# Kernel optimization log

Measured on AMD Instinct MI355X. Metric: run time of the kernel, lower is better.

The kernel has to match this reference:

```python
import jax, jax.numpy as jnp
import numpy as np

N_NODES = 50000
N_EDGES = 600000
IN_CH = 128
OUT_CH = 32
L1 = IN_CH - (IN_CH - OUT_CH) // 3          # 96
L2 = IN_CH - (2 * (IN_CH - OUT_CH)) // 3    # 64


def _lin(key, fan_in, fan_out):
    bound = 1.0 / np.sqrt(fan_in)
    return jax.random.uniform(key, (fan_in, fan_out), jnp.float32, -bound, bound)


def setup_inputs() -> dict:
    key = jax.random.key(0)
    ks = jax.random.split(key, 12)
    x = jax.random.normal(ks[0], (N_NODES, IN_CH), jnp.float32)
    edge_index = jax.random.randint(ks[1], (2, N_EDGES), 0, N_NODES, jnp.int64 if jax.config.jax_enable_x64 else jnp.int32)
    return {
        "x": x,
        "edge_index": edge_index,
        "w1_rel": _lin(ks[2], IN_CH, L1),
        "w1_root": _lin(ks[3], IN_CH, L1),
        "b1": jnp.zeros((L1,), jnp.float32),
        "w2_rel": _lin(ks[4], L1, L2),
        "w2_root": _lin(ks[5], L1, L2),
        "b2": jnp.zeros((L2,), jnp.float32),
        "w_mu": _lin(ks[6], L2, OUT_CH),
        "b_mu": jnp.zeros((OUT_CH,), jnp.float32),
        "w_ls": _lin(ks[7], L2, OUT_CH),
        "b_ls": jnp.zeros((OUT_CH,), jnp.float32),
    }


def reference(x, edge_index, w1_rel, w1_root, b1, w2_rel, w2_root, b2,
              w_mu, b_mu, w_ls, b_ls):
    src, dst = edge_index[0], edge_index[1]

    # PyG GraphConv (aggr='add'): out_i = W_rel @ sum_{j->i} x_j + W_root @ x_i + b
    def graph_conv(h, wr, wroot, b):
        agg = jax.ops.segment_sum(h[src], dst, num_segments=N_NODES)
        return agg @ wr + h @ wroot + b

    h = jax.nn.relu(graph_conv(x, w1_rel, w1_root, b1))
    h = jax.nn.relu(graph_conv(h, w2_rel, w2_root, b2))

    # GCNConv: add self-loops, symmetric deg^-1/2 normalization (shared by mu / logstd)
    loops = jnp.arange(N_NODES, dtype=src.dtype)
    src_sl = jnp.concatenate([src, loops])
    dst_sl = jnp.concatenate([dst, loops])
    deg = jax.ops.segment_sum(jnp.ones_like(dst_sl, h.dtype), dst_sl, num_segments=N_NODES)
    dinv = jnp.where(deg > 0, jax.lax.rsqrt(deg), 0.0)
    norm = dinv[src_sl] * dinv[dst_sl]  # [E+N]

    def gcn(h, w, b):
        m = (h @ w)[src_sl] * norm[:, None]
        return jax.ops.segment_sum(m, dst_sl, num_segments=N_NODES) + b

    return gcn(h, w_mu, b_mu), gcn(h, w_ls, b_ls)
```

## Files before the change

### kernel.cpp

```cpp
#include <hip/hip_runtime.h>
#include <cstddef>

static constexpr int NN = 50000;
static constexpr int NE = 600000;
static constexpr int NB = (NN + 255) / 256;

using f32x4 = __attribute__((ext_vector_type(4))) float;
using s16x8 = __attribute__((ext_vector_type(8))) short;

__device__ inline float bf2f(unsigned short u) {
    return __uint_as_float(((unsigned)u) << 16);
}
__device__ inline unsigned short f2bf(float f) {
    unsigned u = __float_as_uint(f);
    unsigned r = u + 0x7fffu + ((u >> 16) & 1u);
    return (unsigned short)(r >> 16);
}
__device__ inline float lof(unsigned u) { return __uint_as_float(u << 16); }
__device__ inline float hif(unsigned u) { return __uint_as_float(u & 0xffff0000u); }
__device__ inline unsigned packbf(float a, float b) {
    return (unsigned)f2bf(a) | ((unsigned)f2bf(b) << 16);
}

__global__ __launch_bounds__(256)
void zero_wprep_k(int* __restrict__ deg,
                  const float* __restrict__ w1_rel, const float* __restrict__ w1_root,
                  const float* __restrict__ w2_rel, const float* __restrict__ w2_root,
                  const float* __restrict__ w_mu,   const float* __restrict__ w_ls,
                  unsigned short* __restrict__ wt1, unsigned short* __restrict__ wt2,
                  unsigned short* __restrict__ wt3)
{
    int i = blockIdx.x * 256 + threadIdx.x;
    if (i < NN) deg[i] = 0;
    if (i < 24576) {
        int k = i / 192, n = i % 192;
        float v = (n < 96) ? w1_rel[k * 96 + n] : w1_root[k * 96 + (n - 96)];
        wt1[n * 128 + k] = f2bf(v);
    } else if (i < 36864) {
        int j = i - 24576;
        int k = j / 128, n = j % 128;
        float v = (n < 64) ? w2_rel[k * 64 + n] : w2_root[k * 64 + (n - 64)];
        wt2[n * 96 + k] = f2bf(v);
    } else if (i < 40960) {
        int j = i - 36864;
        int k = j / 64, n = j % 64;
        float v = (n < 32) ? w_mu[k * 32 + n] : w_ls[k * 32 + (n - 32)];
        wt3[n * 64 + k] = f2bf(v);
    }
}

__global__ __launch_bounds__(256)
void count_deg_k(const int* __restrict__ dstv, int* __restrict__ deg) {
    int e = blockIdx.x * 256 + threadIdx.x;
    if (e < NE) atomicAdd(&deg[dstv[e]], 1);
}

__global__ __launch_bounds__(256)
void scan_reduce_k(const int* __restrict__ deg, int* __restrict__ partial) {
    __shared__ int buf[256];
    int i = blockIdx.x * 256 + threadIdx.x;
    buf[threadIdx.x] = (i < NN) ? deg[i] : 0;
    __syncthreads();
    #pragma unroll
    for (int off = 128; off > 0; off >>= 1) {
        if (threadIdx.x < off) buf[threadIdx.x] += buf[threadIdx.x + off];
        __syncthreads();
    }
    if (threadIdx.x == 0) partial[blockIdx.x] = buf[0];
}

__global__ __launch_bounds__(256)
void scan_final2_k(const int* __restrict__ deg, const int* __restrict__ partial,
                   int* __restrict__ row_start, int* __restrict__ cursor,
                   float* __restrict__ dinv) {
    __shared__ int pb[256], po[256], buf[256];
    int t = threadIdx.x;
    int pv = (t < NB) ? partial[t] : 0;
    pb[t] = pv; po[t] = pv;
    __syncthreads();
    #pragma unroll
    for (int off = 1; off < 256; off <<= 1) {
        int tv = (t >= off) ? pb[t - off] : 0;
        __syncthreads();
        pb[t] += tv;
        __syncthreads();
    }
    int i = blockIdx.x * 256 + t;
    int v = (i < NN) ? deg[i] : 0;
    buf[t] = v;
    __syncthreads();
    #pragma unroll
    for (int off = 1; off < 256; off <<= 1) {
        int tv = (t >= off) ? buf[t - off] : 0;
        __syncthreads();
        buf[t] += tv;
        __syncthreads();
    }
    int blkoff = pb[blockIdx.x] - po[blockIdx.x];
    if (i < NN) {
        int pos = blkoff + buf[t] - v;
        row_start[i] = pos;
        cursor[i] = pos;
        dinv[i] = rsqrtf((float)v + 1.0f);
    }
    if (blockIdx.x == 0 && t == 0) row_start[NN] = pb[NB - 1];
}

__global__ __launch_bounds__(256)
void fill_k(const int* __restrict__ srcv, const int* __restrict__ dstv,
            int* __restrict__ cursor, int* __restrict__ csr)
{
    int e = blockIdx.x * 256 + threadIdx.x;
    if (e < NE) {
        int pos = atomicAdd(&cursor[dstv[e]], 1);
        csr[pos] = srcv[e];
    }
}

template<int K, int NH, bool XB, bool SCALE>
__global__ __launch_bounds__(256)
void gemm_mfma(const void* __restrict__ Xv,
               const unsigned short* __restrict__ WT,
               const float* __restrict__ biasB,
               const float* __restrict__ scale,
               unsigned short* __restrict__ out0,
               unsigned short* __restrict__ out1)
{
    constexpr int KQ = K / 4;
    constexpr int PB = K * 2;
    constexpr int KS = K / 32;
    constexpr int NT = NH / 16;
    __shared__ short lds[(128 + NH) * K];
    char* ldsb = (char*)lds;
    const int tid = threadIdx.x;
    const int blk = blockIdx.x;
    const int half = blockIdx.y;

    const unsigned short* wt = WT + (size_t)half * NH * K;
    unsigned short* outp = half ? out1 : out0;

    #pragma unroll
    for (int it = 0; it < KQ / 2; ++it) {
        int idx = it * 256 + tid;
        int r = idx / KQ, c4 = idx % KQ;
        int node = blk * 128 + r; if (node >= NN) node = NN - 1;
        uint2 p;
        if (XB) {
            p = *(const uint2*)((const unsigned short*)Xv + (size_t)node * K + c4 * 4);
        } else {
            float4 v = *(const float4*)((const float*)Xv + (size_t)node * K + c4 * 4);
            p.x = packbf(v.x, v.y); p.y = packbf(v.z, v.w);
        }
        unsigned byte = (unsigned)(r * PB + c4 * 8) ^ ((unsigned)(r & 7) << 4);
        *(uint2*)(ldsb + byte) = p;
    }
    #pragma unroll
    for (int it = 0; it < NH * KQ / 256; ++it) {
        int idx = it * 256 + tid;
        int n = idx / KQ, c4 = idx % KQ;
        uint2 p = *(const uint2*)(wt + (size_t)n * K + c4 * 4);
        int pr = 128 + n;
        unsigned byte = (unsigned)(pr * PB + c4 * 8) ^ ((unsigned)(pr & 7) << 4);
        *(uint2*)(ldsb + byte) = p;
    }
    __syncthreads();

    const int wv = tid >> 6, lane = tid & 63;
    const int r15 = lane & 15, g = lane >> 4;

    s16x8 afr[2][KS];
    #pragma unroll
    for (int ms = 0; ms < 2; ++ms) {
        #pragma unroll
        for (int ks = 0; ks < KS; ++ks) {
            int r = wv * 32 + ms * 16 + r15;
            unsigned byte = (unsigned)(r * PB + ks * 64 + g * 16) ^ ((unsigned)(r & 7) << 4);
            afr[ms][ks] = *(const s16x8*)(ldsb + byte);
        }
    }

    #pragma unroll
    for (int nt = 0; nt < NT; ++nt) {
        s16x8 bfr[KS];
        #pragma unroll
        for (int ks = 0; ks < KS; ++ks) {
            int pr = 128 + nt * 16 + r15;
            unsigned byte = (unsigned)(pr * PB + ks * 64 + g * 16) ^ ((unsigned)(pr & 7) << 4);
            bfr[ks] = *(const s16x8*)(ldsb + byte);
        }
        int c = nt * 16 + r15;
        float bias = (half && biasB) ? biasB[c] : 0.f;
        #pragma unroll
        for (int ms = 0; ms < 2; ++ms) {
            f32x4 acc = {0.f, 0.f, 0.f, 0.f};
            #pragma unroll
            for (int ks = 0; ks < KS; ++ks)
                acc = __builtin_amdgcn_mfma_f32_16x16x32_bf16(afr[ms][ks], bfr[ks], acc, 0, 0, 0);
            int nb = blk * 128 + wv * 32 + ms * 16 + g * 4;
            #pragma unroll
            for (int rg = 0; rg < 4; ++rg) {
                int node = nb + rg;
                if (node < NN) {
                    float v = acc[rg] + bias;
                    if (SCALE) v *= scale[node];
                    outp[(size_t)node * NH + c] = f2bf(v);
                }
            }
        }
    }
}

template<int K, int NHT, bool SPLIT, bool SCALE>
__global__ __launch_bounds__(256)
void gather_gemm_k(const int* __restrict__ row_start,
                   const int* __restrict__ csr,
                   const unsigned short* __restrict__ msg,
                   const unsigned short* __restrict__ hpre,
                   const unsigned short* __restrict__ WT,
                   const float* __restrict__ biasHi,
                   const float* __restrict__ scale,
                   unsigned short* __restrict__ out0,
                   unsigned short* __restrict__ out1)
{
    constexpr int G   = K / 8;
    constexpr int KQ  = K / 4;
    constexpr int PB  = K * 2;
    constexpr int KS  = K / 32;
    constexpr int NT  = NHT / 16;
    constexpr int NHh = NHT / 2;
    __shared__ short lds[(64 + NHT) * K];
    char* ldsb = (char*)lds;
    const int tid = threadIdx.x;
    const int blk = blockIdx.x;

    for (int w = tid; w < 64 * G; w += 256) {
        int r = w / G, ch = w - r * G;
        int c8 = ch * 8;
        int node = blk * 64 + r;
        float a[8] = {0.f,0.f,0.f,0.f,0.f,0.f,0.f,0.f};
        if (node < NN) {
            uint4 h = *(const uint4*)&hpre[(size_t)node * K + c8];
            a[0] = lof(h.x); a[1] = hif(h.x); a[2] = lof(h.y); a[3] = hif(h.y);
            a[4] = lof(h.z); a[5] = hif(h.z); a[6] = lof(h.w); a[7] = hif(h.w);
            int e0 = row_start[node], e1 = row_start[node + 1];
            int e = e0;
            for (; e + 2 <= e1; e += 2) {
                int s0 = csr[e], s1 = csr[e + 1];
                uint4 v0 = *(const uint4*)&msg[(size_t)s0 * K + c8];
                uint4 v1 = *(const uint4*)&msg[(size_t)s1 * K + c8];
                a[0] += lof(v0.x); a[1] += hif(v0.x); a[2] += lof(v0.y); a[3] += hif(v0.y);
                a[4] += lof(v0.z); a[5] += hif(v0.z); a[6] += lof(v0.w); a[7] += hif(v0.w);
                a[0] += lof(v1.x); a[1] += hif(v1.x); a[2] += lof(v1.y); a[3] += hif(v1.y);
                a[4] += lof(v1.z); a[5] += hif(v1.z); a[6] += lof(v1.w); a[7] += hif(v1.w);
            }
            if (e < e1) {
                int s = csr[e];
                uint4 v = *(const uint4*)&msg[(size_t)s * K + c8];
                a[0] += lof(v.x); a[1] += hif(v.x); a[2] += lof(v.y); a[3] += hif(v.y);
                a[4] += lof(v.z); a[5] += hif(v.z); a[6] += lof(v.w); a[7] += hif(v.w);
            }
            #pragma unroll
            for (int q = 0; q < 8; ++q) a[q] = fmaxf(a[q], 0.f);
        }
        uint4 o;
        o.x = packbf(a[0], a[1]); o.y = packbf(a[2], a[3]);
        o.z = packbf(a[4], a[5]); o.w = packbf(a[6], a[7]);
        unsigned byte = (unsigned)(r * PB + ch * 16) ^ ((unsigned)(r & 7) << 4);
        *(uint4*)(ldsb + byte) = o;
    }
    #pragma unroll
    for (int it = 0; it < NHT * KQ / 256; ++it) {
        int idx = it * 256 + tid;
        int n = idx / KQ, c4 = idx % KQ;
        uint2 p = *(const uint2*)(WT + (size_t)n * K + c4 * 4);
        int pr = 64 + n;
        unsigned byte = (unsigned)(pr * PB + c4 * 8) ^ ((unsigned)(pr & 7) << 4);
        *(uint2*)(ldsb + byte) = p;
    }
    __syncthreads();

    const int wv = tid >> 6, lane = tid & 63;
    const int r15 = lane & 15, g = lane >> 4;

    s16x8 afr[KS];
    #pragma unroll
    for (int ks = 0; ks < KS; ++ks) {
        int r = wv * 16 + r15;
        unsigned byte = (unsigned)(r * PB + ks * 64 + g * 16) ^ ((unsigned)(r & 7) << 4);
        afr[ks] = *(const s16x8*)(ldsb + byte);
    }

    #pragma unroll
    for (int nt = 0; nt < NT; ++nt) {
        s16x8 bfr[KS];
        #pragma unroll
        for (int ks = 0; ks < KS; ++ks) {
            int pr = 64 + nt * 16 + r15;
            unsigned byte = (unsigned)(pr * PB + ks * 64 + g * 16) ^ ((unsigned)(pr & 7) << 4);
            bfr[ks] = *(const s16x8*)(ldsb + byte);
        }
        int c = nt * 16 + r15;
        float bias = 0.f;
        if (SPLIT && biasHi && c >= NHh) bias = biasHi[c - NHh];
        f32x4 acc = {0.f, 0.f, 0.f, 0.f};
        #pragma unroll
        for (int ks = 0; ks < KS; ++ks)
            acc = __builtin_amdgcn_mfma_f32_16x16x32_bf16(afr[ks], bfr[ks], acc, 0, 0, 0);
        int nb = blk * 64 + wv * 16 + g * 4;
        #pragma unroll
        for (int rg = 0; rg < 4; ++rg) {
            int node = nb + rg;
            if (node < NN) {
                float v = acc[rg] + bias;
                if (SCALE) v *= scale[node];
                if (SPLIT) {
                    if (c < NHh) out0[(size_t)node * NHh + c] = f2bf(v);
                    else         out1[(size_t)node * NHh + (c - NHh)] = f2bf(v);
                } else {
                    out0[(size_t)node * NHT + c] = f2bf(v);
                }
            }
        }
    }
}

__global__ __launch_bounds__(256)
void gather_gcn_k(const int* __restrict__ row_start,
                  const int* __restrict__ csr,
                  const unsigned short* __restrict__ y,
                  const float* __restrict__ dinv,
                  const float* __restrict__ b_mu,
                  const float* __restrict__ b_ls,
                  float* __restrict__ out)
{
    int idx = blockIdx.x * 256 + threadIdx.x;
    if (idx >= NN * 8) return;
    int i  = idx >> 3;
    int c8 = (idx & 7) * 8;
    float a[8];
    {
        uint4 h = *(const uint4*)&y[(size_t)i * 64 + c8];
        a[0] = lof(h.x); a[1] = hif(h.x); a[2] = lof(h.y); a[3] = hif(h.y);
        a[4] = lof(h.z); a[5] = hif(h.z); a[6] = lof(h.w); a[7] = hif(h.w);
    }
    int e0 = row_start[i], e1 = row_start[i + 1];
    int e = e0;
    for (; e + 2 <= e1; e += 2) {
        int s0 = csr[e], s1 = csr[e + 1];
        uint4 v0 = *(const uint4*)&y[(size_t)s0 * 64 + c8];
        uint4 v1 = *(const uint4*)&y[(size_t)s1 * 64 + c8];
        a[0] += lof(v0.x); a[1] += hif(v0.x); a[2] += lof(v0.y); a[3] += hif(v0.y);
        a[4] += lof(v0.z); a[5] += hif(v0.z); a[6] += lof(v0.w); a[7] += hif(v0.w);
        a[0] += lof(v1.x); a[1] += hif(v1.x); a[2] += lof(v1.y); a[3] += hif(v1.y);
        a[4] += lof(v1.z); a[5] += hif(v1.z); a[6] += lof(v1.w); a[7] += hif(v1.w);
    }
    if (e < e1) {
        int s = csr[e];
        uint4 v = *(const uint4*)&y[(size_t)s * 64 + c8];
        a[0] += lof(v.x); a[1] += hif(v.x); a[2] += lof(v.y); a[3] += hif(v.y);
        a[4] += lof(v.z); a[5] += hif(v.z); a[6] += lof(v.w); a[7] += hif(v.w);
    }
    float di = dinv[i];
    const float* b;
    float* o;
    if (c8 < 32) { b = &b_mu[c8];      o = &out[(size_t)i * 32 + c8]; }
    else         { b = &b_ls[c8 - 32]; o = &out[(size_t)NN * 32 + (size_t)i * 32 + (c8 - 32)]; }
    float4 r0, r1;
    r0.x = di * a[0] + b[0]; r0.y = di * a[1] + b[1];
    r0.z = di * a[2] + b[2]; r0.w = di * a[3] + b[3];
    r1.x = di * a[4] + b[4]; r1.y = di * a[5] + b[5];
    r1.z = di * a[6] + b[6]; r1.w = di * a[7] + b[7];
    *(float4*)&o[0] = r0;
    *(float4*)&o[4] = r1;
}

extern "C" void kernel_launch(void* const* d_in, const int* in_sizes, int n_in,
                              void* d_out, int out_size, void* d_ws, size_t ws_size,
                              hipStream_t stream)
{
    (void)in_sizes; (void)n_in; (void)out_size; (void)ws_size;
    const float* x       = (const float*)d_in[0];
    const int*   ei      = (const int*)d_in[1];
    const int*   srcv    = ei;
    const int*   dstv    = ei + NE;
    const float* w1_rel  = (const float*)d_in[2];
    const float* w1_root = (const float*)d_in[3];
    const float* b1      = (const float*)d_in[4];
    const float* w2_rel  = (const float*)d_in[5];
    const float* w2_root = (const float*)d_in[6];
    const float* b2      = (const float*)d_in[7];
    const float* w_mu    = (const float*)d_in[8];
    const float* b_mu    = (const float*)d_in[9];
    const float* w_ls    = (const float*)d_in[10];
    const float* b_ls    = (const float*)d_in[11];
    float* out = (float*)d_out;

    char* ws = (char*)d_ws;
    unsigned short* t1    = (unsigned short*)(ws);
    unsigned short* h1pre = (unsigned short*)(ws + 9600000);
    unsigned short* t2    = (unsigned short*)(ws + 19200000);
    unsigned short* h2pre = (unsigned short*)(ws + 25600000);
    unsigned short* y     = (unsigned short*)(ws + 32000000);
    int* csr       = (int*)(ws + 38400000);
    int* row_start = (int*)(ws + 40800000);
    int* cursor    = (int*)(ws + 41000016);
    float* dinv    = (float*)(ws + 41200016);
    int* deg       = (int*)(ws + 41400016);
    int* partial   = (int*)(ws + 41600016);
    unsigned short* wt1 = (unsigned short*)(ws + 41700016);
    unsigned short* wt2 = (unsigned short*)(ws + 41749168);
    unsigned short* wt3 = (unsigned short*)(ws + 41773744);

    zero_wprep_k<<<NB, 256, 0, stream>>>(deg, w1_rel, w1_root, w2_rel, w2_root,
                                         w_mu, w_ls, wt1, wt2, wt3);
    count_deg_k<<<(NE + 255) / 256, 256, 0, stream>>>(dstv, deg);
    scan_reduce_k<<<NB, 256, 0, stream>>>(deg, partial);
    scan_final2_k<<<NB, 256, 0, stream>>>(deg, partial, row_start, cursor, dinv);
    fill_k<<<(NE + 255) / 256, 256, 0, stream>>>(srcv, dstv, cursor, csr);

    gemm_mfma<128, 96, false, false><<<dim3(391, 2), 256, 0, stream>>>(
        x, wt1, b1, nullptr, t1, h1pre);

    gather_gemm_k<96, 128, true, false><<<782, 256, 0, stream>>>(
        row_start, csr, t1, h1pre, wt2, b2, nullptr, t2, h2pre);

    gather_gemm_k<64, 64, false, true><<<782, 256, 0, stream>>>(
        row_start, csr, t2, h2pre, wt3, nullptr, dinv, y, nullptr);

    gather_gcn_k<<<(NN * 8 + 255) / 256, 256, 0, stream>>>(row_start, csr, y, dinv, b_mu, b_ls, out);
}
```

Baseline: 172.3 us.

## Split neighbor gathers across thread pairs and widen gather-GEMM blocks to 512

```diff
diff --git a/kernel.cpp b/kernel.cpp
--- a/kernel.cpp
+++ b/kernel.cpp
@@ -211,7 +211,7 @@
 }
 
 template<int K, int NHT, bool SPLIT, bool SCALE>
-__global__ __launch_bounds__(256)
+__global__ __launch_bounds__(512)
 void gather_gemm_k(const int* __restrict__ row_start,
                    const int* __restrict__ csr,
                    const unsigned short* __restrict__ msg,
@@ -223,29 +223,36 @@
                    unsigned short* __restrict__ out1)
 {
     constexpr int G   = K / 8;
+    constexpr int G2  = G * 2;
     constexpr int KQ  = K / 4;
     constexpr int PB  = K * 2;
     constexpr int KS  = K / 32;
     constexpr int NT  = NHT / 16;
+    constexpr int NTW = NT / 2;
     constexpr int NHh = NHT / 2;
     __shared__ short lds[(64 + NHT) * K];
     char* ldsb = (char*)lds;
     const int tid = threadIdx.x;
     const int blk = blockIdx.x;
 
-    for (int w = tid; w < 64 * G; w += 256) {
-        int r = w / G, ch = w - r * G;
+    for (int it = 0; it < 64 * G2 / 512; ++it) {
+        int w = it * 512 + tid;
+        int r = w / G2;
+        int rem = w - r * G2;
+        int ch = rem >> 1, sub = rem & 1;
         int c8 = ch * 8;
         int node = blk * 64 + r;
         float a[8] = {0.f,0.f,0.f,0.f,0.f,0.f,0.f,0.f};
         if (node < NN) {
-            uint4 h = *(const uint4*)&hpre[(size_t)node * K + c8];
-            a[0] = lof(h.x); a[1] = hif(h.x); a[2] = lof(h.y); a[3] = hif(h.y);
-            a[4] = lof(h.z); a[5] = hif(h.z); a[6] = lof(h.w); a[7] = hif(h.w);
+            if (sub == 0) {
+                uint4 h = *(const uint4*)&hpre[(size_t)node * K + c8];
+                a[0] = lof(h.x); a[1] = hif(h.x); a[2] = lof(h.y); a[3] = hif(h.y);
+                a[4] = lof(h.z); a[5] = hif(h.z); a[6] = lof(h.w); a[7] = hif(h.w);
+            }
             int e0 = row_start[node], e1 = row_start[node + 1];
-            int e = e0;
-            for (; e + 2 <= e1; e += 2) {
-                int s0 = csr[e], s1 = csr[e + 1];
+            int e = e0 + sub;
+            for (; e + 2 < e1; e += 4) {
+                int s0 = csr[e], s1 = csr[e + 2];
                 uint4 v0 = *(const uint4*)&msg[(size_t)s0 * K + c8];
                 uint4 v1 = *(const uint4*)&msg[(size_t)s1 * K + c8];
                 a[0] += lof(v0.x); a[1] += hif(v0.x); a[2] += lof(v0.y); a[3] += hif(v0.y);
@@ -259,18 +266,23 @@
                 a[0] += lof(v.x); a[1] += hif(v.x); a[2] += lof(v.y); a[3] += hif(v.y);
                 a[4] += lof(v.z); a[5] += hif(v.z); a[6] += lof(v.w); a[7] += hif(v.w);
             }
-            #pragma unroll
-            for (int q = 0; q < 8; ++q) a[q] = fmaxf(a[q], 0.f);
-        }
-        uint4 o;
-        o.x = packbf(a[0], a[1]); o.y = packbf(a[2], a[3]);
-        o.z = packbf(a[4], a[5]); o.w = packbf(a[6], a[7]);
-        unsigned byte = (unsigned)(r * PB + ch * 16) ^ ((unsigned)(r & 7) << 4);
-        *(uint4*)(ldsb + byte) = o;
-    }
-    #pragma unroll
-    for (int it = 0; it < NHT * KQ / 256; ++it) {
-        int idx = it * 256 + tid;
+        }
+        #pragma unroll
+        for (int q = 0; q < 8; ++q) {
+            a[q] += __shfl_xor(a[q], 1);
+            a[q] = fmaxf(a[q], 0.f);
+        }
+        if (sub == 0) {
+            uint4 o;
+            o.x = packbf(a[0], a[1]); o.y = packbf(a[2], a[3]);
+            o.z = packbf(a[4], a[5]); o.w = packbf(a[6], a[7]);
+            unsigned byte = (unsigned)(r * PB + ch * 16) ^ ((unsigned)(r & 7) << 4);
+            *(uint4*)(ldsb + byte) = o;
+        }
+    }
+    #pragma unroll
+    for (int it = 0; it < NHT * KQ / 512; ++it) {
+        int idx = it * 512 + tid;
         int n = idx / KQ, c4 = idx % KQ;
         uint2 p = *(const uint2*)(WT + (size_t)n * K + c4 * 4);
         int pr = 64 + n;
@@ -281,17 +293,19 @@
 
     const int wv = tid >> 6, lane = tid & 63;
     const int r15 = lane & 15, g = lane >> 4;
+    const int rt = wv >> 1, nth = wv & 1;
 
     s16x8 afr[KS];
     #pragma unroll
     for (int ks = 0; ks < KS; ++ks) {
-        int r = wv * 16 + r15;
+        int r = rt * 16 + r15;
         unsigned byte = (unsigned)(r * PB + ks * 64 + g * 16) ^ ((unsigned)(r & 7) << 4);
         afr[ks] = *(const s16x8*)(ldsb + byte);
     }
 
     #pragma unroll
-    for (int nt = 0; nt < NT; ++nt) {
+    for (int ntl = 0; ntl < NTW; ++ntl) {
+        int nt = nth * NTW + ntl;
         s16x8 bfr[KS];
         #pragma unroll
         for (int ks = 0; ks < KS; ++ks) {
@@ -306,7 +320,7 @@
         #pragma unroll
         for (int ks = 0; ks < KS; ++ks)
             acc = __builtin_amdgcn_mfma_f32_16x16x32_bf16(afr[ks], bfr[ks], acc, 0, 0, 0);
-        int nb = blk * 64 + wv * 16 + g * 4;
+        int nb = blk * 64 + rt * 16 + g * 4;
         #pragma unroll
         for (int rg = 0; rg < 4; ++rg) {
             int node = nb + rg;
@@ -334,19 +348,20 @@
                   float* __restrict__ out)
 {
     int idx = blockIdx.x * 256 + threadIdx.x;
-    if (idx >= NN * 8) return;
-    int i  = idx >> 3;
-    int c8 = (idx & 7) * 8;
-    float a[8];
-    {
+    int i   = idx >> 4;
+    int rem = idx & 15;
+    int ch = rem >> 1, sub = rem & 1;
+    int c8 = ch * 8;
+    float a[8] = {0.f,0.f,0.f,0.f,0.f,0.f,0.f,0.f};
+    if (sub == 0) {
         uint4 h = *(const uint4*)&y[(size_t)i * 64 + c8];
         a[0] = lof(h.x); a[1] = hif(h.x); a[2] = lof(h.y); a[3] = hif(h.y);
         a[4] = lof(h.z); a[5] = hif(h.z); a[6] = lof(h.w); a[7] = hif(h.w);
     }
     int e0 = row_start[i], e1 = row_start[i + 1];
-    int e = e0;
-    for (; e + 2 <= e1; e += 2) {
-        int s0 = csr[e], s1 = csr[e + 1];
+    int e = e0 + sub;
+    for (; e + 2 < e1; e += 4) {
+        int s0 = csr[e], s1 = csr[e + 2];
         uint4 v0 = *(const uint4*)&y[(size_t)s0 * 64 + c8];
         uint4 v1 = *(const uint4*)&y[(size_t)s1 * 64 + c8];
         a[0] += lof(v0.x); a[1] += hif(v0.x); a[2] += lof(v0.y); a[3] += hif(v0.y);
@@ -360,6 +375,9 @@
         a[0] += lof(v.x); a[1] += hif(v.x); a[2] += lof(v.y); a[3] += hif(v.y);
         a[4] += lof(v.z); a[5] += hif(v.z); a[6] += lof(v.w); a[7] += hif(v.w);
     }
+    #pragma unroll
+    for (int q = 0; q < 8; ++q) a[q] += __shfl_xor(a[q], 1);
+    if (sub) return;
     float di = dinv[i];
     const float* b;
     float* o;
@@ -421,11 +439,11 @@
     gemm_mfma<128, 96, false, false><<<dim3(391, 2), 256, 0, stream>>>(
         x, wt1, b1, nullptr, t1, h1pre);
 
-    gather_gemm_k<96, 128, true, false><<<782, 256, 0, stream>>>(
+    gather_gemm_k<96, 128, true, false><<<782, 512, 0, stream>>>(
         row_start, csr, t1, h1pre, wt2, b2, nullptr, t2, h2pre);
 
-    gather_gemm_k<64, 64, false, true><<<782, 256, 0, stream>>>(
+    gather_gemm_k<64, 64, false, true><<<782, 512, 0, stream>>>(
         row_start, csr, t2, h2pre, wt3, nullptr, dinv, y, nullptr);
 
-    gather_gcn_k<<<(NN * 8 + 255) / 256, 256, 0, stream>>>(row_start, csr, y, dinv, b_mu, b_ls, out);
-}
+    gather_gcn_k<<<(NN * 16) / 256, 256, 0, stream>>>(row_start, csr, y, dinv, b_mu, b_ls, out);
+}
```

New measurement: 159.2 us, median of 2. 7.6% less time.
